# Kernel tuning notes

Hardware: AMD Instinct MI355X
Metric: run time of the kernel (lower is better)

Reference implementation:

```python
import jax, jax.numpy as jnp
import numpy as np

DIM = 2048
N_HEADS = 16
HEAD_DIM = 128
EPS = 1e-6


def setup_inputs() -> dict:
    key = jax.random.key(0)
    ks = jax.random.split(key, 8)
    b, gf, gh, gw = 1, 8, 16, 24
    s = gf * gh * gw
    c = HEAD_DIM // 2
    w = lambda k: 0.02 * jax.random.normal(k, (DIM, DIM), jnp.float32)
    return {
        "x": jax.random.normal(ks[0], (b, s, DIM), jnp.float32),
        "freqs_angle": jax.random.normal(ks[1], (1024, c), jnp.float32),
        "Wq": w(ks[2]), "bq": jnp.zeros((DIM,), jnp.float32),
        "Wk": w(ks[3]), "bk": jnp.zeros((DIM,), jnp.float32),
        "Wv": w(ks[4]), "bv": jnp.zeros((DIM,), jnp.float32),
        "Wo": w(ks[5]), "bo": jnp.zeros((DIM,), jnp.float32),
        "gq": jnp.ones((DIM,), jnp.float32),
        "gk": jnp.ones((DIM,), jnp.float32),
        "seq_len": s, "grid_f": gf, "grid_h": gh, "grid_w": gw,
    }


def _rms(t, g):
    return t * jax.lax.rsqrt(jnp.mean(t * t, axis=-1, keepdims=True) + EPS) * g


def _grid_angles(freqs_angle, gf, gh, gw, c):
    # band split [c - 2*(c//3), c//3, c//3] as in rope_apply
    cf = c - 2 * (c // 3)
    ch = cw = c // 3
    af = freqs_angle[:gf, :cf]            # [F, cf]
    ah = freqs_angle[:gh, cf:cf + ch]     # [H, ch]
    aw = freqs_angle[:gw, cf + ch:c]      # [W, cw]
    ang = jnp.concatenate([
        jnp.broadcast_to(af[:, None, None, :], (gf, gh, gw, cf)),
        jnp.broadcast_to(ah[None, :, None, :], (gf, gh, gw, ch)),
        jnp.broadcast_to(aw[None, None, :, :], (gf, gh, gw, cw)),
    ], axis=-1)
    return ang.reshape(gf * gh * gw, c)   # [s, c]


def reference(x, freqs_angle, Wq, bq, Wk, bk, Wv, bv, Wo, bo, gq, gk,
              seq_len, grid_f, grid_h, grid_w):
    b, s, _ = x.shape
    n, d = N_HEADS, HEAD_DIM
    c = d // 2
    ang = _grid_angles(freqs_angle, grid_f, grid_h, grid_w, c)
    cos = jnp.cos(ang)[None, :, None, :]  # [1, s, 1, c]
    sin = jnp.sin(ang)[None, :, None, :]

    def rope(t):  # complex multiply on (even, odd) = (real, imag) pairs
        te, to = t[..., 0::2], t[..., 1::2]
        return jnp.stack([te * cos - to * sin, te * sin + to * cos], axis=-1).reshape(t.shape)

    q = _rms(x @ Wq.T + bq, gq).reshape(b, s, n, d)
    k = _rms(x @ Wk.T + bk, gk).reshape(b, s, n, d)
    v = (x @ Wv.T + bv).reshape(b, s, n, d)
    q, k = rope(q), rope(k)

    scale = np.float32(1.0 / np.sqrt(d))
    scores = jnp.einsum('bqnd,bknd->bnqk', q, k) * scale
    p = jax.nn.softmax(scores, axis=-1)
    o = jnp.einsum('bnqk,bknd->bqnd', p, v).reshape(b, s, n * d)
    return o @ Wo.T + bo
```

## Files before the change

### kernel.cpp

```cpp
#include <hip/hip_runtime.h>
#include <stdint.h>
#include <stddef.h>

typedef __bf16 bf16_t;
typedef __bf16 bf16x8 __attribute__((ext_vector_type(8)));
typedef __bf16 bf16x4 __attribute__((ext_vector_type(4)));
typedef __bf16 bf16x2 __attribute__((ext_vector_type(2)));
typedef float  f32x4  __attribute__((ext_vector_type(4)));

#define SEQ   3072
#define DIMD  2048
#define NH    16
#define HD    128
#define QKVN  6144

__device__ __forceinline__ void async16(const bf16_t* g, bf16_t* l) {
  __builtin_amdgcn_global_load_lds((const __attribute__((address_space(1))) uint32_t*)g,
                                   (__attribute__((address_space(3))) uint32_t*)l, 16, 0, 0);
}

__global__ __launch_bounds__(256) void cvt_all(const float* __restrict__ x,
                                               const float* __restrict__ Wq,
                                               const float* __restrict__ Wk,
                                               const float* __restrict__ Wv,
                                               const float* __restrict__ Wo,
                                               const float* __restrict__ bq,
                                               const float* __restrict__ bk,
                                               const float* __restrict__ bv,
                                               bf16_t* __restrict__ xb,
                                               bf16_t* __restrict__ Wqkvb,
                                               bf16_t* __restrict__ Wob,
                                               float* __restrict__ bqkv) {
  const int b = blockIdx.x;
  const float* src; bf16_t* dst; int off;
  if (b < 3072)       { src = x;  dst = xb;              off = b; }
  else if (b < 5120)  { src = Wq; dst = Wqkvb;           off = b - 3072; }
  else if (b < 7168)  { src = Wk; dst = Wqkvb + 4194304; off = b - 5120; }
  else if (b < 9216)  { src = Wv; dst = Wqkvb + 8388608; off = b - 7168; }
  else if (b < 11264) { src = Wo; dst = Wob;             off = b - 9216; }
  else {
    int t = (b - 11264) * 256 + threadIdx.x;
    float v;
    if (t < 2048)      v = bq[t];
    else if (t < 4096) v = bk[t - 2048];
    else               v = bv[t - 4096];
    bqkv[t] = v;
    return;
  }
  const int idx = (off * 256 + threadIdx.x) * 8;
  const float4 a = *(const float4*)(src + idx);
  const float4 c = *(const float4*)(src + idx + 4);
  bf16x8 o;
  o[0] = (bf16_t)a.x; o[1] = (bf16_t)a.y; o[2] = (bf16_t)a.z; o[3] = (bf16_t)a.w;
  o[4] = (bf16_t)c.x; o[5] = (bf16_t)c.y; o[6] = (bf16_t)c.z; o[7] = (bf16_t)c.w;
  *(bf16x8*)(dst + idx) = o;
}

template<bool OUT_BF16>
__global__ __launch_bounds__(256, 3) void gemm_nt(const bf16_t* __restrict__ A,
                                                  const bf16_t* __restrict__ B,
                                                  const float* __restrict__ bias,
                                                  void* __restrict__ Cout,
                                                  int M, int N, int K) {
  __shared__ __align__(16) bf16_t As[128 * 64];
  __shared__ __align__(16) bf16_t Bs[128 * 64];
  const int t = threadIdx.x;
  const int lane = t & 63, wave = t >> 6;
  const int quad = lane >> 4, l15 = lane & 15;
  const int wy = wave >> 1, wx = wave & 1;
  const size_t bm = (size_t)blockIdx.y * 128, bn = (size_t)blockIdx.x * 128;
  const bf16_t* Ab = A + bm * K;
  const bf16_t* Bb = B + bn * K;
  f32x4 acc[4][4] = {};
  int srow[4], scol[4];
#pragma unroll
  for (int r = 0; r < 4; r++) {
    int L = r * 256 + t;
    int row = L >> 3, cp = L & 7;
    srow[r] = row;
    scol[r] = (cp ^ (row & 7)) * 8;
  }
  for (int k0 = 0; k0 < K; k0 += 64) {
    __syncthreads();
#pragma unroll
    for (int r = 0; r < 4; r++)
      async16(Ab + (size_t)srow[r] * K + k0 + scol[r], &As[(r * 256 + t) * 8]);
#pragma unroll
    for (int r = 0; r < 4; r++)
      async16(Bb + (size_t)srow[r] * K + k0 + scol[r], &Bs[(r * 256 + t) * 8]);
    __syncthreads();
#pragma unroll
    for (int ks = 0; ks < 2; ks++) {
      bf16x8 af[4], bfv[4];
#pragma unroll
      for (int i = 0; i < 4; i++) {
        int row = wy * 64 + i * 16 + l15;
        af[i] = *(const bf16x8*)&As[row * 64 + (((ks * 4 + quad) ^ (row & 7)) * 8)];
      }
#pragma unroll
      for (int j = 0; j < 4; j++) {
        int row = wx * 64 + j * 16 + l15;
        bfv[j] = *(const bf16x8*)&Bs[row * 64 + (((ks * 4 + quad) ^ (row & 7)) * 8)];
      }
#pragma unroll
      for (int i = 0; i < 4; i++)
#pragma unroll
        for (int j = 0; j < 4; j++)
          acc[i][j] = __builtin_amdgcn_mfma_f32_16x16x32_bf16(af[i], bfv[j], acc[i][j], 0, 0, 0);
    }
  }
#pragma unroll
  for (int i = 0; i < 4; i++) {
#pragma unroll
    for (int j = 0; j < 4; j++) {
      size_t row = bm + wy * 64 + i * 16 + quad * 4;
      size_t col = bn + wx * 64 + j * 16 + l15;
      float bb = bias[col];
#pragma unroll
      for (int r = 0; r < 4; r++) {
        float v = acc[i][j][r] + bb;
        if (OUT_BF16) ((bf16_t*)Cout)[(row + r) * N + col] = (bf16_t)v;
        else          ((float*)Cout)[(row + r) * N + col] = v;
      }
    }
  }
}

template<bool OUT_BF16>
__global__ __launch_bounds__(256, 3) void gemm_nt64(const bf16_t* __restrict__ A,
                                                    const bf16_t* __restrict__ B,
                                                    const float* __restrict__ bias,
                                                    void* __restrict__ Cout,
                                                    int M, int N, int K) {
  __shared__ __align__(16) bf16_t As[128 * 64];
  __shared__ __align__(16) bf16_t Bs[64 * 64];
  const int t = threadIdx.x;
  const int lane = t & 63, wave = t >> 6;
  const int quad = lane >> 4, l15 = lane & 15;
  const int wy = wave >> 1, wx = wave & 1;
  const size_t bm = (size_t)blockIdx.y * 128, bn = (size_t)blockIdx.x * 64;
  const bf16_t* Ab = A + bm * K;
  const bf16_t* Bb = B + bn * K;
  f32x4 acc[4][2] = {};
  for (int k0 = 0; k0 < K; k0 += 64) {
    __syncthreads();
#pragma unroll
    for (int r = 0; r < 4; r++) {
      int L = r * 256 + t, row = L >> 3, cp = L & 7;
      async16(Ab + (size_t)row * K + k0 + (cp ^ (row & 7)) * 8, &As[L * 8]);
    }
#pragma unroll
    for (int r = 0; r < 2; r++) {
      int L = r * 256 + t, row = L >> 3, cp = L & 7;
      async16(Bb + (size_t)row * K + k0 + (cp ^ (row & 7)) * 8, &Bs[L * 8]);
    }
    __syncthreads();
#pragma unroll
    for (int ks = 0; ks < 2; ks++) {
      bf16x8 af[4], bfv[2];
#pragma unroll
      for (int i = 0; i < 4; i++) {
        int row = wy * 64 + i * 16 + l15;
        af[i] = *(const bf16x8*)&As[row * 64 + (((ks * 4 + quad) ^ (row & 7)) * 8)];
      }
#pragma unroll
      for (int j = 0; j < 2; j++) {
        int row = wx * 32 + j * 16 + l15;
        bfv[j] = *(const bf16x8*)&Bs[row * 64 + (((ks * 4 + quad) ^ (row & 7)) * 8)];
      }
#pragma unroll
      for (int i = 0; i < 4; i++)
#pragma unroll
        for (int j = 0; j < 2; j++)
          acc[i][j] = __builtin_amdgcn_mfma_f32_16x16x32_bf16(af[i], bfv[j], acc[i][j], 0, 0, 0);
    }
  }
#pragma unroll
  for (int i = 0; i < 4; i++) {
#pragma unroll
    for (int j = 0; j < 2; j++) {
      size_t row = bm + wy * 64 + i * 16 + quad * 4;
      size_t col = bn + wx * 32 + j * 16 + l15;
      float bb = bias[col];
#pragma unroll
      for (int r = 0; r < 4; r++) {
        float v = acc[i][j][r] + bb;
        if (OUT_BF16) ((bf16_t*)Cout)[(row + r) * N + col] = (bf16_t)v;
        else          ((float*)Cout)[(row + r) * N + col] = v;
      }
    }
  }
}

__global__ __launch_bounds__(256) void rmsrope(bf16_t* __restrict__ qkv,
                                               bf16_t* __restrict__ pk,
                                               const float* __restrict__ gq,
                                               const float* __restrict__ gk,
                                               const float* __restrict__ freqs) {
  const int s = blockIdx.x, t = threadIdx.x;
  const float SC2 = 0.08838834764831845f * 1.44269504088896f;
  bf16_t* row = qkv + (size_t)s * QKVN;
  bf16x8 qv = *(const bf16x8*)&row[t * 8];
  bf16x8 kv = *(const bf16x8*)&row[2048 + t * 8];
  float qf[8], kf[8];
  float qs = 0.f, ks2 = 0.f;
#pragma unroll
  for (int i = 0; i < 8; i++) {
    qf[i] = (float)qv[i]; qs  += qf[i] * qf[i];
    kf[i] = (float)kv[i]; ks2 += kf[i] * kf[i];
  }
#pragma unroll
  for (int m = 1; m < 64; m <<= 1) {
    qs  += __shfl_xor(qs, m);
    ks2 += __shfl_xor(ks2, m);
  }
  __shared__ float red[2][4];
  const int wave = t >> 6, lane = t & 63;
  if (lane == 0) { red[0][wave] = qs; red[1][wave] = ks2; }
  __syncthreads();
  qs  = red[0][0] + red[0][1] + red[0][2] + red[0][3];
  ks2 = red[1][0] + red[1][1] + red[1][2] + red[1][3];
  const float qsc = rsqrtf(qs  / 2048.f + 1e-6f) * SC2;
  const float ksc = rsqrtf(ks2 / 2048.f + 1e-6f);
  const int sf = s / 384, rem = s - sf * 384;
  const int sh = rem / 24, sw = rem - sh * 24;
  bf16x8 qo, ko;
#pragma unroll
  for (int u = 0; u < 4; u++) {
    const int col = t * 8 + 2 * u;
    const int i = (col >> 1) & 63;
    const int frow = (i < 22) ? sf : ((i < 43) ? sh : sw);
    const float ang = freqs[frow * 64 + i];
    float sn, cs;
    __sincosf(ang, &sn, &cs);
    float te = qf[2 * u]     * qsc * gq[col];
    float to = qf[2 * u + 1] * qsc * gq[col + 1];
    qo[2 * u]     = (bf16_t)(te * cs - to * sn);
    qo[2 * u + 1] = (bf16_t)(te * sn + to * cs);
    te = kf[2 * u]     * ksc * gk[col];
    to = kf[2 * u + 1] * ksc * gk[col + 1];
    ko[2 * u]     = (bf16_t)(te * cs - to * sn);
    ko[2 * u + 1] = (bf16_t)(te * sn + to * cs);
  }
  *(bf16x8*)&row[t * 8] = qo;
  *(bf16x8*)&pk[((size_t)(t >> 4) * SEQ + s) * HD + (t & 15) * 8] = ko;
}

__global__ __launch_bounds__(256) void vtrans(const bf16_t* __restrict__ qkv,
                                              bf16_t* __restrict__ pvt) {
  __shared__ bf16_t tile[128][65];
  const int h = blockIdx.y;
  const int s0 = blockIdx.x * 64;
  const int t = threadIdx.x;
#pragma unroll
  for (int r = 0; r < 4; r++) {
    int L = r * 256 + t, s = L >> 4, cp = L & 15;
    bf16x8 v = *(const bf16x8*)&qkv[(size_t)(s0 + s) * QKVN + 4096 + h * HD + cp * 8];
#pragma unroll
    for (int i = 0; i < 8; i++) tile[cp * 8 + i][s] = v[i];
  }
  __syncthreads();
#pragma unroll
  for (int r = 0; r < 4; r++) {
    int L = r * 256 + t, d = L >> 3, c = L & 7;
    bf16x8 o;
#pragma unroll
    for (int i = 0; i < 8; i++) o[i] = tile[d][c * 8 + i];
    *(bf16x8*)&pvt[((size_t)h * HD + d) * SEQ + s0 + c * 8] = o;
  }
}

__global__ __launch_bounds__(256, 2) void flash_attn(const bf16_t* __restrict__ qkv,
                                                     const bf16_t* __restrict__ pk,
                                                     const bf16_t* __restrict__ pvt,
                                                     bf16_t* __restrict__ ob) {
  __shared__ __align__(16) bf16_t Ks[2][64 * 128];
  __shared__ __align__(16) bf16_t Vt[2][128 * 64];
  __shared__ __align__(16) bf16_t Ps[4][32 * 64];
  const int h = blockIdx.y, qt = blockIdx.x;
  const int s0 = qt * 128;
  const int t = threadIdx.x, wave = t >> 6, lane = t & 63;
  const int quad = lane >> 4, l15 = lane & 15;
  const int wq = wave * 32;
  const bf16_t* pkh = pk  + (size_t)h * (SEQ * HD);
  const bf16_t* pvh = pvt + (size_t)h * (HD * SEQ);
  int krow4[4], kc4[4], vd4[4], vc4[4];
#pragma unroll
  for (int r = 0; r < 4; r++) {
    int L = r * 256 + t;
    krow4[r] = L >> 4; kc4[r] = (L & 15) ^ (krow4[r] & 7);
    vd4[r]   = L >> 3; vc4[r] = (L & 7)  ^ (vd4[r] & 7);
  }
  bf16x8 qfr[2][4];
#pragma unroll
  for (int tj = 0; tj < 2; tj++)
#pragma unroll
    for (int ks = 0; ks < 4; ks++)
      qfr[tj][ks] = *(const bf16x8*)&qkv[(size_t)(s0 + wq + tj * 16 + l15) * QKVN + h * HD + ks * 32 + quad * 8];
  bf16x8 onesf;
#pragma unroll
  for (int i = 0; i < 8; i++) onesf[i] = (bf16_t)1.0f;
  f32x4 oacc[2][8] = {};
  f32x4 lacc[2] = {};
  float m_run[2] = {-3e38f, -3e38f};
#pragma unroll
  for (int r = 0; r < 4; r++) {
    int L = r * 256 + t;
    async16(pkh + (size_t)krow4[r] * HD + kc4[r] * 8, &Ks[0][L * 8]);
  }
#pragma unroll
  for (int r = 0; r < 4; r++) {
    int L = r * 256 + t;
    async16(pvh + (size_t)vd4[r] * SEQ + vc4[r] * 8, &Vt[0][L * 8]);
  }
  for (int kt = 0; kt < SEQ / 64; kt++) {
    const int cur = kt & 1;
    __syncthreads();
    if (kt + 1 < SEQ / 64) {
      const int kv1 = (kt + 1) * 64;
#pragma unroll
      for (int r = 0; r < 4; r++) {
        int L = r * 256 + t;
        async16(pkh + (size_t)(kv1 + krow4[r]) * HD + kc4[r] * 8, &Ks[cur ^ 1][L * 8]);
      }
#pragma unroll
      for (int r = 0; r < 4; r++) {
        int L = r * 256 + t;
        async16(pvh + (size_t)vd4[r] * SEQ + kv1 + vc4[r] * 8, &Vt[cur ^ 1][L * 8]);
      }
    }
    f32x4 st[4][2] = {};
#pragma unroll
    for (int ks = 0; ks < 4; ks++) {
      bf16x8 kfr[4];
#pragma unroll
      for (int ti = 0; ti < 4; ti++) {
        const int kr = ti * 16 + l15;
        kfr[ti] = *(const bf16x8*)&Ks[cur][kr * 128 + (((ks * 4 + quad) ^ (kr & 7)) * 8)];
      }
#pragma unroll
      for (int ti = 0; ti < 4; ti++)
#pragma unroll
        for (int tj = 0; tj < 2; tj++)
          st[ti][tj] = __builtin_amdgcn_mfma_f32_16x16x32_bf16(kfr[ti], qfr[tj][ks], st[ti][tj], 0, 0, 0);
    }
    float mt[2] = {-3e38f, -3e38f};
#pragma unroll
    for (int ti = 0; ti < 4; ti++)
#pragma unroll
      for (int tj = 0; tj < 2; tj++)
#pragma unroll
        for (int r = 0; r < 4; r++)
          mt[tj] = fmaxf(mt[tj], st[ti][tj][r]);
    float al[2];
#pragma unroll
    for (int tj = 0; tj < 2; tj++) {
      mt[tj] = fmaxf(mt[tj], __shfl_xor(mt[tj], 16));
      mt[tj] = fmaxf(mt[tj], __shfl_xor(mt[tj], 32));
      const float mn = fmaxf(m_run[tj], mt[tj]);
      al[tj] = exp2f(m_run[tj] - mn);
      m_run[tj] = mn;
    }
#pragma unroll
    for (int ti = 0; ti < 4; ti++)
#pragma unroll
      for (int tj = 0; tj < 2; tj++) {
        bf16x4 pv;
#pragma unroll
        for (int r = 0; r < 4; r++)
          pv[r] = (bf16_t)exp2f(st[ti][tj][r] - m_run[tj]);
        const int q = tj * 16 + l15;
        const int cp2 = (ti * 2 + (quad >> 1)) ^ (q & 7);
        *(bf16x4*)&Ps[wave][q * 64 + cp2 * 8 + (quad & 1) * 4] = pv;
      }
    if (__ballot((al[0] != 1.f) | (al[1] != 1.f))) {
#pragma unroll
      for (int ti = 0; ti < 2; ti++) {
        float a0 = __shfl(al[ti], quad * 4 + 0);
        float a1 = __shfl(al[ti], quad * 4 + 1);
        float a2 = __shfl(al[ti], quad * 4 + 2);
        float a3 = __shfl(al[ti], quad * 4 + 3);
        lacc[ti][0] *= a0; lacc[ti][1] *= a1;
        lacc[ti][2] *= a2; lacc[ti][3] *= a3;
#pragma unroll
        for (int dj = 0; dj < 8; dj++) {
          oacc[ti][dj][0] *= a0; oacc[ti][dj][1] *= a1;
          oacc[ti][dj][2] *= a2; oacc[ti][dj][3] *= a3;
        }
      }
    }
#pragma unroll
    for (int ks = 0; ks < 2; ks++) {
      bf16x8 pf[2], vf[8];
#pragma unroll
      for (int ti = 0; ti < 2; ti++) {
        const int q = ti * 16 + l15;
        pf[ti] = *(const bf16x8*)&Ps[wave][q * 64 + (((ks * 4 + quad) ^ (q & 7)) * 8)];
      }
#pragma unroll
      for (int dj = 0; dj < 8; dj++) {
        const int d = dj * 16 + l15;
        vf[dj] = *(const bf16x8*)&Vt[cur][d * 64 + (((ks * 4 + quad) ^ (d & 7)) * 8)];
      }
#pragma unroll
      for (int ti = 0; ti < 2; ti++) {
        lacc[ti] = __builtin_amdgcn_mfma_f32_16x16x32_bf16(pf[ti], onesf, lacc[ti], 0, 0, 0);
#pragma unroll
        for (int dj = 0; dj < 8; dj++)
          oacc[ti][dj] = __builtin_amdgcn_mfma_f32_16x16x32_bf16(pf[ti], vf[dj], oacc[ti][dj], 0, 0, 0);
      }
    }
  }
#pragma unroll
  for (int ti = 0; ti < 2; ti++) {
    float li[4];
#pragma unroll
    for (int r = 0; r < 4; r++) li[r] = 1.f / lacc[ti][r];
#pragma unroll
    for (int dj = 0; dj < 8; dj++)
#pragma unroll
      for (int r = 0; r < 4; r++) {
        const float v = oacc[ti][dj][r] * li[r];
        ob[(size_t)(s0 + wq + ti * 16 + quad * 4 + r) * DIMD + h * HD + dj * 16 + l15] = (bf16_t)v;
      }
  }
}

extern "C" void kernel_launch(void* const* d_in, const int* in_sizes, int n_in,
                              void* d_out, int out_size, void* d_ws, size_t ws_size,
                              hipStream_t stream) {
  (void)in_sizes; (void)n_in; (void)out_size;
  const float* x     = (const float*)d_in[0];
  const float* freqs = (const float*)d_in[1];
  const float* Wq    = (const float*)d_in[2];
  const float* bq    = (const float*)d_in[3];
  const float* Wk    = (const float*)d_in[4];
  const float* bk    = (const float*)d_in[5];
  const float* Wv    = (const float*)d_in[6];
  const float* bv    = (const float*)d_in[7];
  const float* Wo    = (const float*)d_in[8];
  const float* bo    = (const float*)d_in[9];
  const float* gq    = (const float*)d_in[10];
  const float* gk    = (const float*)d_in[11];

  char* w = (char*)d_ws;
  bf16_t* xb    = (bf16_t*)(w);
  bf16_t* Wqkvb = (bf16_t*)(w + 12582912);
  bf16_t* Wob   = (bf16_t*)(w + 37748736);
  bf16_t* qkvb  = (bf16_t*)(w + 46137344);
  bf16_t* obuf  = (bf16_t*)(w + 83886080);
  float*  bqkv  = (float*) (w + 96468992);
  bf16_t* pk    = (bf16_t*)(w);
  bf16_t* pvt   = (bf16_t*)(w + 12582912);
  if (ws_size < (size_t)96493568) return;

  cvt_all<<<11288, 256, 0, stream>>>(x, Wq, Wk, Wv, Wo, bq, bk, bv, xb, Wqkvb, Wob, bqkv);

  gemm_nt<true><<<dim3(48, 24), 256, 0, stream>>>(xb, Wqkvb, bqkv, qkvb, SEQ, QKVN, DIMD);
  rmsrope<<<3072, 256, 0, stream>>>(qkvb, pk, gq, gk, freqs);
  vtrans<<<dim3(48, NH), 256, 0, stream>>>(qkvb, pvt);
  flash_attn<<<dim3(24, NH), 256, 0, stream>>>(qkvb, pk, pvt, obuf);
  gemm_nt64<false><<<dim3(32, 24), 256, 0, stream>>>(obuf, Wob, bo, (float*)d_out, SEQ, DIMD, DIMD);
}
```

Baseline: 438.4 us.

## Merge rmsrope and V-transpose kernels; give each attention wave 64 query rows

The RMSNorm+RoPE kernel and the V transpose kernel become a single launch, with the extra blocks doing the transpose, which saves one launch and its tail. Flash attention moves from 4 waves of 32 query rows to 2 waves of 64 rows per block (128 threads). Each K/V fragment read from LDS is now reused across twice as many query tiles. The cost is doubled accumulator registers per wave and only 384 blocks of 2 waves each, so occupancy drops and latency hiding may suffer.

```diff
diff --git a/kernel.cpp b/kernel.cpp
--- a/kernel.cpp
+++ b/kernel.cpp
@@ -192,12 +192,37 @@
   }
 }
 
-__global__ __launch_bounds__(256) void rmsrope(bf16_t* __restrict__ qkv,
-                                               bf16_t* __restrict__ pk,
-                                               const float* __restrict__ gq,
-                                               const float* __restrict__ gk,
-                                               const float* __restrict__ freqs) {
-  const int s = blockIdx.x, t = threadIdx.x;
+__global__ __launch_bounds__(256) void prep(bf16_t* __restrict__ qkv,
+                                            bf16_t* __restrict__ pk,
+                                            bf16_t* __restrict__ pvt,
+                                            const float* __restrict__ gq,
+                                            const float* __restrict__ gk,
+                                            const float* __restrict__ freqs) {
+  __shared__ bf16_t tile[128][65];
+  const int t = threadIdx.x;
+  if (blockIdx.x >= 3072) {
+    const int vb = blockIdx.x - 3072;
+    const int h = vb / 48;
+    const int s0 = (vb - h * 48) * 64;
+#pragma unroll
+    for (int r = 0; r < 4; r++) {
+      int L = r * 256 + t, s = L >> 4, cp = L & 15;
+      bf16x8 v = *(const bf16x8*)&qkv[(size_t)(s0 + s) * QKVN + 4096 + h * HD + cp * 8];
+#pragma unroll
+      for (int i = 0; i < 8; i++) tile[cp * 8 + i][s] = v[i];
+    }
+    __syncthreads();
+#pragma unroll
+    for (int r = 0; r < 4; r++) {
+      int L = r * 256 + t, d = L >> 3, c = L & 7;
+      bf16x8 o;
+#pragma unroll
+      for (int i = 0; i < 8; i++) o[i] = tile[d][c * 8 + i];
+      *(bf16x8*)&pvt[((size_t)h * HD + d) * SEQ + s0 + c * 8] = o;
+    }
+    return;
+  }
+  const int s = blockIdx.x;
   const float SC2 = 0.08838834764831845f * 1.44269504088896f;
   bf16_t* row = qkv + (size_t)s * QKVN;
   bf16x8 qv = *(const bf16x8*)&row[t * 8];
@@ -246,90 +271,60 @@
   *(bf16x8*)&pk[((size_t)(t >> 4) * SEQ + s) * HD + (t & 15) * 8] = ko;
 }
 
-__global__ __launch_bounds__(256) void vtrans(const bf16_t* __restrict__ qkv,
-                                              bf16_t* __restrict__ pvt) {
-  __shared__ bf16_t tile[128][65];
-  const int h = blockIdx.y;
-  const int s0 = blockIdx.x * 64;
-  const int t = threadIdx.x;
-#pragma unroll
-  for (int r = 0; r < 4; r++) {
-    int L = r * 256 + t, s = L >> 4, cp = L & 15;
-    bf16x8 v = *(const bf16x8*)&qkv[(size_t)(s0 + s) * QKVN + 4096 + h * HD + cp * 8];
-#pragma unroll
-    for (int i = 0; i < 8; i++) tile[cp * 8 + i][s] = v[i];
-  }
-  __syncthreads();
-#pragma unroll
-  for (int r = 0; r < 4; r++) {
-    int L = r * 256 + t, d = L >> 3, c = L & 7;
-    bf16x8 o;
-#pragma unroll
-    for (int i = 0; i < 8; i++) o[i] = tile[d][c * 8 + i];
-    *(bf16x8*)&pvt[((size_t)h * HD + d) * SEQ + s0 + c * 8] = o;
-  }
-}
-
-__global__ __launch_bounds__(256, 2) void flash_attn(const bf16_t* __restrict__ qkv,
+__global__ __launch_bounds__(128, 1) void flash_attn(const bf16_t* __restrict__ qkv,
                                                      const bf16_t* __restrict__ pk,
                                                      const bf16_t* __restrict__ pvt,
                                                      bf16_t* __restrict__ ob) {
   __shared__ __align__(16) bf16_t Ks[2][64 * 128];
   __shared__ __align__(16) bf16_t Vt[2][128 * 64];
-  __shared__ __align__(16) bf16_t Ps[4][32 * 64];
+  __shared__ __align__(16) bf16_t Ps[2][64 * 64];
   const int h = blockIdx.y, qt = blockIdx.x;
   const int s0 = qt * 128;
   const int t = threadIdx.x, wave = t >> 6, lane = t & 63;
   const int quad = lane >> 4, l15 = lane & 15;
-  const int wq = wave * 32;
+  const int wq = wave * 64;
   const bf16_t* pkh = pk  + (size_t)h * (SEQ * HD);
   const bf16_t* pvh = pvt + (size_t)h * (HD * SEQ);
-  int krow4[4], kc4[4], vd4[4], vc4[4];
-#pragma unroll
-  for (int r = 0; r < 4; r++) {
-    int L = r * 256 + t;
-    krow4[r] = L >> 4; kc4[r] = (L & 15) ^ (krow4[r] & 7);
-    vd4[r]   = L >> 3; vc4[r] = (L & 7)  ^ (vd4[r] & 7);
-  }
-  bf16x8 qfr[2][4];
-#pragma unroll
-  for (int tj = 0; tj < 2; tj++)
+  int koff[8], voff[8];
+#pragma unroll
+  for (int r = 0; r < 8; r++) {
+    int L = r * 128 + t;
+    int krow = L >> 4, kc = (L & 15) ^ (krow & 7);
+    koff[r] = krow * HD + kc * 8;
+    int vd = L >> 3, vc = (L & 7) ^ (vd & 7);
+    voff[r] = vd * SEQ + vc * 8;
+  }
+  bf16x8 qfr[4][4];
+#pragma unroll
+  for (int tj = 0; tj < 4; tj++)
 #pragma unroll
     for (int ks = 0; ks < 4; ks++)
       qfr[tj][ks] = *(const bf16x8*)&qkv[(size_t)(s0 + wq + tj * 16 + l15) * QKVN + h * HD + ks * 32 + quad * 8];
   bf16x8 onesf;
 #pragma unroll
   for (int i = 0; i < 8; i++) onesf[i] = (bf16_t)1.0f;
-  f32x4 oacc[2][8] = {};
-  f32x4 lacc[2] = {};
-  float m_run[2] = {-3e38f, -3e38f};
-#pragma unroll
-  for (int r = 0; r < 4; r++) {
-    int L = r * 256 + t;
-    async16(pkh + (size_t)krow4[r] * HD + kc4[r] * 8, &Ks[0][L * 8]);
-  }
-#pragma unroll
-  for (int r = 0; r < 4; r++) {
-    int L = r * 256 + t;
-    async16(pvh + (size_t)vd4[r] * SEQ + vc4[r] * 8, &Vt[0][L * 8]);
-  }
+  f32x4 oacc[4][8] = {};
+  f32x4 lacc[4] = {};
+  float m_run[4] = {-3e38f, -3e38f, -3e38f, -3e38f};
+#pragma unroll
+  for (int r = 0; r < 8; r++)
+    async16(pkh + koff[r], &Ks[0][(r * 128 + t) * 8]);
+#pragma unroll
+  for (int r = 0; r < 8; r++)
+    async16(pvh + voff[r], &Vt[0][(r * 128 + t) * 8]);
   for (int kt = 0; kt < SEQ / 64; kt++) {
     const int cur = kt & 1;
     __syncthreads();
     if (kt + 1 < SEQ / 64) {
       const int kv1 = (kt + 1) * 64;
 #pragma unroll
-      for (int r = 0; r < 4; r++) {
-        int L = r * 256 + t;
-        async16(pkh + (size_t)(kv1 + krow4[r]) * HD + kc4[r] * 8, &Ks[cur ^ 1][L * 8]);
-      }
-#pragma unroll
-      for (int r = 0; r < 4; r++) {
-        int L = r * 256 + t;
-        async16(pvh + (size_t)vd4[r] * SEQ + kv1 + vc4[r] * 8, &Vt[cur ^ 1][L * 8]);
-      }
-    }
-    f32x4 st[4][2] = {};
+      for (int r = 0; r < 8; r++)
+        async16(pkh + (size_t)kv1 * HD + koff[r], &Ks[cur ^ 1][(r * 128 + t) * 8]);
+#pragma unroll
+      for (int r = 0; r < 8; r++)
+        async16(pvh + kv1 + voff[r], &Vt[cur ^ 1][(r * 128 + t) * 8]);
+    }
+    f32x4 st[4][4] = {};
 #pragma unroll
     for (int ks = 0; ks < 4; ks++) {
       bf16x8 kfr[4];
@@ -341,20 +336,20 @@
 #pragma unroll
       for (int ti = 0; ti < 4; ti++)
 #pragma unroll
-        for (int tj = 0; tj < 2; tj++)
+        for (int tj = 0; tj < 4; tj++)
           st[ti][tj] = __builtin_amdgcn_mfma_f32_16x16x32_bf16(kfr[ti], qfr[tj][ks], st[ti][tj], 0, 0, 0);
     }
-    float mt[2] = {-3e38f, -3e38f};
+    float mt[4] = {-3e38f, -3e38f, -3e38f, -3e38f};
 #pragma unroll
     for (int ti = 0; ti < 4; ti++)
 #pragma unroll
-      for (int tj = 0; tj < 2; tj++)
+      for (int tj = 0; tj < 4; tj++)
 #pragma unroll
         for (int r = 0; r < 4; r++)
           mt[tj] = fmaxf(mt[tj], st[ti][tj][r]);
-    float al[2];
-#pragma unroll
-    for (int tj = 0; tj < 2; tj++) {
+    float al[4];
+#pragma unroll
+    for (int tj = 0; tj < 4; tj++) {
       mt[tj] = fmaxf(mt[tj], __shfl_xor(mt[tj], 16));
       mt[tj] = fmaxf(mt[tj], __shfl_xor(mt[tj], 32));
       const float mn = fmaxf(m_run[tj], mt[tj]);
@@ -364,7 +359,7 @@
 #pragma unroll
     for (int ti = 0; ti < 4; ti++)
 #pragma unroll
-      for (int tj = 0; tj < 2; tj++) {
+      for (int tj = 0; tj < 4; tj++) {
         bf16x4 pv;
 #pragma unroll
         for (int r = 0; r < 4; r++)
@@ -373,29 +368,29 @@
         const int cp2 = (ti * 2 + (quad >> 1)) ^ (q & 7);
         *(bf16x4*)&Ps[wave][q * 64 + cp2 * 8 + (quad & 1) * 4] = pv;
       }
-    if (__ballot((al[0] != 1.f) | (al[1] != 1.f))) {
-#pragma unroll
-      for (int ti = 0; ti < 2; ti++) {
-        float a0 = __shfl(al[ti], quad * 4 + 0);
-        float a1 = __shfl(al[ti], quad * 4 + 1);
-        float a2 = __shfl(al[ti], quad * 4 + 2);
-        float a3 = __shfl(al[ti], quad * 4 + 3);
-        lacc[ti][0] *= a0; lacc[ti][1] *= a1;
-        lacc[ti][2] *= a2; lacc[ti][3] *= a3;
+    if (__ballot((al[0] != 1.f) | (al[1] != 1.f) | (al[2] != 1.f) | (al[3] != 1.f))) {
+#pragma unroll
+      for (int tq = 0; tq < 4; tq++) {
+        float a0 = __shfl(al[tq], quad * 4 + 0);
+        float a1 = __shfl(al[tq], quad * 4 + 1);
+        float a2 = __shfl(al[tq], quad * 4 + 2);
+        float a3 = __shfl(al[tq], quad * 4 + 3);
+        lacc[tq][0] *= a0; lacc[tq][1] *= a1;
+        lacc[tq][2] *= a2; lacc[tq][3] *= a3;
 #pragma unroll
         for (int dj = 0; dj < 8; dj++) {
-          oacc[ti][dj][0] *= a0; oacc[ti][dj][1] *= a1;
-          oacc[ti][dj][2] *= a2; oacc[ti][dj][3] *= a3;
+          oacc[tq][dj][0] *= a0; oacc[tq][dj][1] *= a1;
+          oacc[tq][dj][2] *= a2; oacc[tq][dj][3] *= a3;
         }
       }
     }
 #pragma unroll
     for (int ks = 0; ks < 2; ks++) {
-      bf16x8 pf[2], vf[8];
-#pragma unroll
-      for (int ti = 0; ti < 2; ti++) {
-        const int q = ti * 16 + l15;
-        pf[ti] = *(const bf16x8*)&Ps[wave][q * 64 + (((ks * 4 + quad) ^ (q & 7)) * 8)];
+      bf16x8 pf[4], vf[8];
+#pragma unroll
+      for (int tq = 0; tq < 4; tq++) {
+        const int q = tq * 16 + l15;
+        pf[tq] = *(const bf16x8*)&Ps[wave][q * 64 + (((ks * 4 + quad) ^ (q & 7)) * 8)];
       }
 #pragma unroll
       for (int dj = 0; dj < 8; dj++) {
@@ -403,25 +398,25 @@
         vf[dj] = *(const bf16x8*)&Vt[cur][d * 64 + (((ks * 4 + quad) ^ (d & 7)) * 8)];
       }
 #pragma unroll
-      for (int ti = 0; ti < 2; ti++) {
-        lacc[ti] = __builtin_amdgcn_mfma_f32_16x16x32_bf16(pf[ti], onesf, lacc[ti], 0, 0, 0);
+      for (int tq = 0; tq < 4; tq++) {
+        lacc[tq] = __builtin_amdgcn_mfma_f32_16x16x32_bf16(pf[tq], onesf, lacc[tq], 0, 0, 0);
 #pragma unroll
         for (int dj = 0; dj < 8; dj++)
-          oacc[ti][dj] = __builtin_amdgcn_mfma_f32_16x16x32_bf16(pf[ti], vf[dj], oacc[ti][dj], 0, 0, 0);
-      }
-    }
-  }
-#pragma unroll
-  for (int ti = 0; ti < 2; ti++) {
+          oacc[tq][dj] = __builtin_amdgcn_mfma_f32_16x16x32_bf16(pf[tq], vf[dj], oacc[tq][dj], 0, 0, 0);
+      }
+    }
+  }
+#pragma unroll
+  for (int tq = 0; tq < 4; tq++) {
     float li[4];
 #pragma unroll
-    for (int r = 0; r < 4; r++) li[r] = 1.f / lacc[ti][r];
+    for (int r = 0; r < 4; r++) li[r] = 1.f / lacc[tq][r];
 #pragma unroll
     for (int dj = 0; dj < 8; dj++)
 #pragma unroll
       for (int r = 0; r < 4; r++) {
-        const float v = oacc[ti][dj][r] * li[r];
-        ob[(size_t)(s0 + wq + ti * 16 + quad * 4 + r) * DIMD + h * HD + dj * 16 + l15] = (bf16_t)v;
+        const float v = oacc[tq][dj][r] * li[r];
+        ob[(size_t)(s0 + wq + tq * 16 + quad * 4 + r) * DIMD + h * HD + dj * 16 + l15] = (bf16_t)v;
       }
   }
 }
@@ -457,8 +452,7 @@
   cvt_all<<<11288, 256, 0, stream>>>(x, Wq, Wk, Wv, Wo, bq, bk, bv, xb, Wqkvb, Wob, bqkv);
 
   gemm_nt<true><<<dim3(48, 24), 256, 0, stream>>>(xb, Wqkvb, bqkv, qkvb, SEQ, QKVN, DIMD);
-  rmsrope<<<3072, 256, 0, stream>>>(qkvb, pk, gq, gk, freqs);
-  vtrans<<<dim3(48, NH), 256, 0, stream>>>(qkvb, pvt);
-  flash_attn<<<dim3(24, NH), 256, 0, stream>>>(qkvb, pk, pvt, obuf);
+  prep<<<3840, 256, 0, stream>>>(qkvb, pk, pvt, gq, gk, freqs);
+  flash_attn<<<dim3(24, NH), 128, 0, stream>>>(qkvb, pk, pvt, obuf);
   gemm_nt64<false><<<dim3(32, 24), 256, 0, stream>>>(obuf, Wob, bo, (float*)d_out, SEQ, DIMD, DIMD);
 }
```

Measured after the change: 512.2 us. 16.8% more time.
